# Performance work log

Measured on AMD Instinct MI355X. Metric: run time of the kernel, lower is better.

## Reference

```python
import jax, jax.numpy as jnp
import numpy as np

N_NODES = 100000
N_EDGES = 1600000
IN_FEATS, HIDDEN, OUT_MU, OUT_LV = 256, 128, 64, 64


def setup_inputs() -> dict:
    key = jax.random.key(0)
    ks = jax.random.split(key, 8)
    X = jax.random.normal(ks[0], (N_NODES, IN_FEATS), dtype=jnp.float32)
    edge_index = jax.random.randint(ks[1], (2, N_EDGES), 0, N_NODES, dtype=jnp.int64)
    def glorot(k, shape):
        lim = np.sqrt(6.0 / (shape[0] + shape[1])).astype(np.float32)
        return jax.random.uniform(k, shape, jnp.float32, -lim, lim)
    W1 = glorot(ks[2], (IN_FEATS, HIDDEN))
    b1 = jnp.zeros((HIDDEN,), jnp.float32)
    Wmu = glorot(ks[3], (HIDDEN, OUT_MU))
    bmu = jnp.zeros((OUT_MU,), jnp.float32)
    Wlv = glorot(ks[4], (HIDDEN, OUT_LV))
    blv = jnp.zeros((OUT_LV,), jnp.float32)
    return {"X": X, "edge_index": edge_index, "W1": W1, "b1": b1,
            "Wmu": Wmu, "bmu": bmu, "Wlv": Wlv, "blv": blv}


def _gcn_norm(edge_index, num_nodes):
    # Add self-loops (PyG GCNConv default) and compute symmetric normalization.
    loop = jnp.arange(num_nodes, dtype=edge_index.dtype)
    row = jnp.concatenate([edge_index[0], loop])  # source
    col = jnp.concatenate([edge_index[1], loop])  # target
    deg = jax.ops.segment_sum(jnp.ones_like(col, dtype=jnp.float32), col,
                              num_segments=num_nodes)
    dinv = jnp.where(deg > 0, jax.lax.rsqrt(deg), 0.0)
    norm = dinv[row] * dinv[col]  # [E+N]
    return row, col, norm


def _gcn_conv(x, W, b, row, col, norm, num_nodes):
    # Linear transform, then normalized sparse neighbor aggregation at targets.
    h = x @ W                                   # [N, F_out]
    msg = h[row] * norm[:, None]                # gather + scale, [E+N, F_out]
    out = jax.ops.segment_sum(msg, col, num_segments=num_nodes)
    return out + b


def reference(X, edge_index, W1, b1, Wmu, bmu, Wlv, blv):
    n = X.shape[0]
    row, col, norm = _gcn_norm(edge_index, n)
    H = jax.nn.relu(_gcn_conv(X, W1, b1, row, col, norm, n))
    mu = _gcn_conv(H, Wmu, bmu, row, col, norm, n)
    lv = _gcn_conv(H, Wlv, blv, row, col, norm, n)
    return (mu, lv)
```

## Files before the change

### kernel.cpp

```cpp
#include <hip/hip_runtime.h>
#include <hip/hip_bf16.h>
#include <cstdint>

#define N_FEATS_IN 256
#define HID 128
#define OUTF 64
#define SITEMS 8
#define NXCD 8

typedef __bf16 bf16x8 __attribute__((ext_vector_type(8)));
typedef __bf16 bf16x2 __attribute__((ext_vector_type(2)));
typedef float f32x4 __attribute__((ext_vector_type(4)));

__device__ __forceinline__ int xcc_id() {
  int x;
  asm volatile("s_getreg_b32 %0, hwreg(HW_REG_XCC_ID, 0, 32)" : "=s"(x));
  return x & (NXCD - 1);
}


__global__ __launch_bounds__(256) void count_deg_kernel(const int* __restrict__ ei, int E,
    int N, int* __restrict__ cnt8, int* __restrict__ erank) {
  int e = blockIdx.x * 256 + threadIdx.x;
  int x = xcc_id();
  if (e < E) {
    int c = ei[E + e];
    int lr = __hip_atomic_fetch_add(&cnt8[(size_t)x * N + c], 1,
                                    __ATOMIC_RELAXED, __HIP_MEMORY_SCOPE_WORKGROUP);
    erank[e] = lr | (x << 28);
  }
}

__global__ __launch_bounds__(256) void combine_kernel(int* __restrict__ cnt8,
    int* __restrict__ deg, float* __restrict__ dinv, int n) {
  int c = blockIdx.x * 256 + threadIdx.x;
  if (c < n) {
    int s = 0;
#pragma unroll
    for (int x = 0; x < NXCD; ++x) {
      int v = cnt8[(size_t)x * n + c];
      cnt8[(size_t)x * n + c] = s;
      s += v;
    }
    deg[c] = s;
    dinv[c] = rsqrtf((float)(s + 1));
  }
}


__global__ __launch_bounds__(256) void scan_part_kernel(const int* __restrict__ cnt, int n,
                                                        int* __restrict__ bsum) {
  __shared__ int ts[256];
  const int t = threadIdx.x;
  int base = (blockIdx.x * 256 + t) * SITEMS;
  int s = 0;
#pragma unroll
  for (int i = 0; i < SITEMS; ++i) {
    int idx = base + i;
    if (idx < n) s += cnt[idx];
  }
  ts[t] = s;
  __syncthreads();
  for (int off = 128; off > 0; off >>= 1) {
    if (t < off) ts[t] += ts[t + off];
    __syncthreads();
  }
  if (t == 0) bsum[blockIdx.x] = ts[0];
}

__global__ __launch_bounds__(256) void scan_bsum_kernel(int* __restrict__ bsum, int nb) {
  __shared__ int ts[256];
  const int t = threadIdx.x;
  int v = (t < nb) ? bsum[t] : 0;
  ts[t] = v;
  __syncthreads();
  for (int off = 1; off < 256; off <<= 1) {
    int u = (t >= off) ? ts[t - off] : 0;
    __syncthreads();
    ts[t] += u;
    __syncthreads();
  }
  if (t < nb) bsum[t] = ts[t] - v;
}

__global__ __launch_bounds__(256) void scan_final_kernel(const int* __restrict__ cnt, int n,
    const int* __restrict__ bsum, int* __restrict__ ptr) {
  __shared__ int ts[256];
  const int t = threadIdx.x;
  int base = (blockIdx.x * 256 + t) * SITEMS;
  int loc[SITEMS];
  int s = 0;
#pragma unroll
  for (int i = 0; i < SITEMS; ++i) {
    int idx = base + i;
    loc[i] = (idx < n) ? cnt[idx] : 0;
    s += loc[i];
  }
  ts[t] = s;
  __syncthreads();
  for (int off = 1; off < 256; off <<= 1) {
    int u = (t >= off) ? ts[t - off] : 0;
    __syncthreads();
    ts[t] += u;
    __syncthreads();
  }
  int run = bsum[blockIdx.x] + ts[t] - s;
#pragma unroll
  for (int i = 0; i < SITEMS; ++i) {
    int idx = base + i;
    if (idx < n) ptr[idx] = run;
    run += loc[i];
  }
  if (base < n && base + SITEMS >= n) ptr[n] = run;
}


__global__ __launch_bounds__(256) void fill_kernel(const int* __restrict__ ei, int E, int N,
    const int* __restrict__ ptr, const int* __restrict__ offs, const int* __restrict__ erank,
    const float* __restrict__ dinv, int2* __restrict__ erec) {
  int e = blockIdx.x * 256 + threadIdx.x;
  if (e < E) {
    int r = ei[e];
    int c = ei[E + e];
    int er = erank[e];
    int x = er >> 28;
    int lr = er & 0x0FFFFFFF;
    int pos = ptr[c] + offs[(size_t)x * N + c] + lr;
    int2 rec;
    rec.x = r;
    rec.y = __float_as_int(dinv[r] * dinv[c]);
    erec[pos] = rec;
  }
}


__global__ __launch_bounds__(256) void pack_all_kernel(const float* __restrict__ W1,
    const float* __restrict__ Wmu, const float* __restrict__ Wlv,
    __bf16* __restrict__ W1p, __bf16* __restrict__ Wcp) {
  int idx = blockIdx.x * 256 + threadIdx.x;
  if (idx < 32768) {
    int j = idx & 7, l = (idx >> 3) & 63, t = (idx >> 9) & 7, s = idx >> 12;
    int k = s * 32 + (l >> 4) * 8 + j;
    int n = t * 16 + (l & 15);
    W1p[idx] = (__bf16)W1[k * HID + n];
  } else if (idx < 49152) {
    int i2 = idx - 32768;
    int j = i2 & 7, l = (i2 >> 3) & 63, t = (i2 >> 9) & 7, s = i2 >> 12;
    int k = s * 32 + (l >> 4) * 8 + j;
    int g = t * 16 + (l & 15);
    float v = (g < OUTF) ? Wmu[k * OUTF + g] : Wlv[k * OUTF + (g - OUTF)];
    Wcp[i2] = (__bf16)v;
  }
}


__global__ __launch_bounds__(256) void gemm1_mfma(const float* __restrict__ X,
    const __bf16* __restrict__ Wp, __bf16* __restrict__ Yb, int nrows, int ntiles) {
  __shared__ __bf16 bs[32768];
  const int tid = threadIdx.x;
  {
    const float4* s4 = (const float4*)Wp;
    float4* d4 = (float4*)bs;
#pragma unroll
    for (int i = 0; i < 16; ++i) d4[tid + 256 * i] = s4[tid + 256 * i];
  }
  __syncthreads();
  const int lane = tid & 63;
  const int wave = tid >> 6;
  const int lm = lane & 15;
  const int q = lane >> 4;
  const bf16x8* bsv = (const bf16x8*)bs;

  for (int tile = blockIdx.x; tile < ntiles; tile += gridDim.x) {
    const int rb = tile * 128 + wave * 32;
    int r0 = min(rb + lm, nrows - 1);
    int r1 = min(rb + 16 + lm, nrows - 1);
    const float* x0 = X + (size_t)r0 * N_FEATS_IN + q * 8;
    const float* x1 = X + (size_t)r1 * N_FEATS_IN + q * 8;

    f32x4 acc[2][8];
#pragma unroll
    for (int m = 0; m < 2; ++m)
#pragma unroll
      for (int t = 0; t < 8; ++t) acc[m][t] = (f32x4)0.f;

#pragma unroll
    for (int s = 0; s < 8; ++s) {
      float4 u0 = ((const float4*)(x0 + s * 32))[0];
      float4 v0 = ((const float4*)(x0 + s * 32))[1];
      float4 u1 = ((const float4*)(x1 + s * 32))[0];
      float4 v1 = ((const float4*)(x1 + s * 32))[1];
      bf16x8 a0, a1;
      a0[0] = (__bf16)u0.x; a0[1] = (__bf16)u0.y; a0[2] = (__bf16)u0.z; a0[3] = (__bf16)u0.w;
      a0[4] = (__bf16)v0.x; a0[5] = (__bf16)v0.y; a0[6] = (__bf16)v0.z; a0[7] = (__bf16)v0.w;
      a1[0] = (__bf16)u1.x; a1[1] = (__bf16)u1.y; a1[2] = (__bf16)u1.z; a1[3] = (__bf16)u1.w;
      a1[4] = (__bf16)v1.x; a1[5] = (__bf16)v1.y; a1[6] = (__bf16)v1.z; a1[7] = (__bf16)v1.w;
#pragma unroll
      for (int t = 0; t < 8; ++t) {
        bf16x8 b = bsv[(s * 8 + t) * 64 + lane];
        acc[0][t] = __builtin_amdgcn_mfma_f32_16x16x32_bf16(a0, b, acc[0][t], 0, 0, 0);
        acc[1][t] = __builtin_amdgcn_mfma_f32_16x16x32_bf16(a1, b, acc[1][t], 0, 0, 0);
      }
    }
#pragma unroll
    for (int m = 0; m < 2; ++m) {
      int rowbase = rb + m * 16 + q * 4;
#pragma unroll
      for (int t = 0; t < 8; ++t) {
#pragma unroll
        for (int r = 0; r < 4; ++r) {
          int row = rowbase + r;
          if (row < nrows) Yb[(size_t)row * HID + t * 16 + lm] = (__bf16)acc[m][t][r];
        }
      }
    }
  }
}


__global__ __launch_bounds__(64) void agg_kernel(const __bf16* __restrict__ Fin,
    const int* __restrict__ ptr, const int2* __restrict__ erec,
    const float* __restrict__ dinv, const float* __restrict__ bias,
    __bf16* __restrict__ Fout, int do_relu) {
  const int c = blockIdx.x;
  const int t = threadIdx.x;
  const float d = dinv[c];
  bf16x2 sv = ((const bf16x2*)(Fin + (size_t)c * HID))[t];
  float ax = d * d * (float)sv[0];
  float ay = d * d * (float)sv[1];
  const int beg = ptr[c], end = ptr[c + 1];
  int e = beg;
  for (; e + 4 <= end; e += 4) {
    int2 p0 = erec[e], p1 = erec[e + 1], p2 = erec[e + 2], p3 = erec[e + 3];
    float n0 = __int_as_float(p0.y), n1 = __int_as_float(p1.y);
    float n2 = __int_as_float(p2.y), n3 = __int_as_float(p3.y);
    bf16x2 v0 = ((const bf16x2*)(Fin + (size_t)p0.x * HID))[t];
    bf16x2 v1 = ((const bf16x2*)(Fin + (size_t)p1.x * HID))[t];
    bf16x2 v2 = ((const bf16x2*)(Fin + (size_t)p2.x * HID))[t];
    bf16x2 v3 = ((const bf16x2*)(Fin + (size_t)p3.x * HID))[t];
    ax = fmaf(n0, (float)v0[0], ax); ay = fmaf(n0, (float)v0[1], ay);
    ax = fmaf(n1, (float)v1[0], ax); ay = fmaf(n1, (float)v1[1], ay);
    ax = fmaf(n2, (float)v2[0], ax); ay = fmaf(n2, (float)v2[1], ay);
    ax = fmaf(n3, (float)v3[0], ax); ay = fmaf(n3, (float)v3[1], ay);
  }
  for (; e < end; ++e) {
    int2 p = erec[e];
    float nn = __int_as_float(p.y);
    bf16x2 v = ((const bf16x2*)(Fin + (size_t)p.x * HID))[t];
    ax = fmaf(nn, (float)v[0], ax);
    ay = fmaf(nn, (float)v[1], ay);
  }
  if (do_relu) {
    ax = fmaxf(ax + bias[2 * t], 0.f);
    ay = fmaxf(ay + bias[2 * t + 1], 0.f);
  }
  bf16x2 o;
  o[0] = (__bf16)ax;
  o[1] = (__bf16)ay;
  ((bf16x2*)(Fout + (size_t)c * HID))[t] = o;
}


__global__ __launch_bounds__(256) void gemm2_mfma(const __bf16* __restrict__ Gb,
    const __bf16* __restrict__ Wp, const float* __restrict__ bmu,
    const float* __restrict__ blv, float* __restrict__ out, int nrows) {
  __shared__ __bf16 bs[16384];
  const int tid = threadIdx.x;
  {
    const float4* s4 = (const float4*)Wp;
    float4* d4 = (float4*)bs;
#pragma unroll
    for (int i = 0; i < 8; ++i) d4[tid + 256 * i] = s4[tid + 256 * i];
  }
  __syncthreads();
  const int lane = tid & 63;
  const int wave = tid >> 6;
  const int rb = blockIdx.x * 128 + wave * 32;
  const int lm = lane & 15;
  const int q = lane >> 4;
  const bf16x8* bsv = (const bf16x8*)bs;

  f32x4 acc[2][8];
#pragma unroll
  for (int m = 0; m < 2; ++m)
#pragma unroll
    for (int t = 0; t < 8; ++t) acc[m][t] = (f32x4)0.f;

  int r0 = min(rb + lm, nrows - 1);
  int r1 = min(rb + 16 + lm, nrows - 1);
  const __bf16* g0 = Gb + (size_t)r0 * HID + q * 8;
  const __bf16* g1 = Gb + (size_t)r1 * HID + q * 8;

#pragma unroll
  for (int s = 0; s < 4; ++s) {
    bf16x8 a0 = *(const bf16x8*)(g0 + s * 32);
    bf16x8 a1 = *(const bf16x8*)(g1 + s * 32);
#pragma unroll
    for (int t = 0; t < 8; ++t) {
      bf16x8 b = bsv[(s * 8 + t) * 64 + lane];
      acc[0][t] = __builtin_amdgcn_mfma_f32_16x16x32_bf16(a0, b, acc[0][t], 0, 0, 0);
      acc[1][t] = __builtin_amdgcn_mfma_f32_16x16x32_bf16(a1, b, acc[1][t], 0, 0, 0);
    }
  }
#pragma unroll
  for (int m = 0; m < 2; ++m) {
    int rowbase = rb + m * 16 + q * 4;
#pragma unroll
    for (int t = 0; t < 8; ++t) {
      int g = t * 16 + lm;
      float bv = (g < OUTF) ? bmu[g] : blv[g - OUTF];
      float* ob = (g < OUTF) ? (out + g) : (out + (size_t)nrows * OUTF + (g - OUTF));
#pragma unroll
      for (int r = 0; r < 4; ++r) {
        int row = rowbase + r;
        if (row < nrows) ob[(size_t)row * OUTF] = acc[m][t][r] + bv;
      }
    }
  }
}


extern "C" void kernel_launch(void* const* d_in, const int* in_sizes, int n_in,
                              void* d_out, int out_size, void* d_ws, size_t ws_size,
                              hipStream_t stream) {
  const float* X   = (const float*)d_in[0];
  const int*   ei  = (const int*)d_in[1];
  const float* W1  = (const float*)d_in[2];
  const float* b1  = (const float*)d_in[3];
  const float* Wmu = (const float*)d_in[4];
  const float* bmu = (const float*)d_in[5];
  const float* Wlv = (const float*)d_in[6];
  const float* blv = (const float*)d_in[7];
  float* out = (float*)d_out;

  const int N = in_sizes[0] / N_FEATS_IN;
  const int E = in_sizes[1] / 2;

  char* ws = (char*)d_ws;
  size_t off = 0;
  auto alloc = [&](size_t bytes) -> void* {
    void* p = ws + off;
    off += (bytes + 255) & ~(size_t)255;
    return p;
  };
  __bf16* Yb  = (__bf16*)alloc((size_t)N * HID * 2);
  __bf16* Hb  = (__bf16*)alloc((size_t)N * HID * 2);
  float* dinv = (float*)alloc((size_t)N * 4);
  int*   deg  = (int*)alloc((size_t)N * 4);
  int*   ptr  = (int*)alloc((size_t)(N + 1) * 4);
  int*   cnt8 = (int*)alloc((size_t)NXCD * N * 4);
  int*   erank = (int*)alloc((size_t)E * 4);
  int2*  erec = (int2*)alloc((size_t)E * 8);
  __bf16* W1p = (__bf16*)alloc(32768 * 2);
  __bf16* Wcp = (__bf16*)alloc(16384 * 2);
  int*   bsum = (int*)alloc(256 * 4);
  (void)ws_size; (void)n_in; (void)out_size;

  hipMemsetAsync(cnt8, 0, (size_t)NXCD * N * 4, stream);

  int ge = (E + 255) / 256;
  int gn = (N + 255) / 256;
  int nb = (N + 256 * SITEMS - 1) / (256 * SITEMS);
  count_deg_kernel<<<ge, 256, 0, stream>>>(ei, E, N, cnt8, erank);
  combine_kernel<<<gn, 256, 0, stream>>>(cnt8, deg, dinv, N);
  scan_part_kernel<<<nb, 256, 0, stream>>>(deg, N, bsum);
  scan_bsum_kernel<<<1, 256, 0, stream>>>(bsum, nb);
  scan_final_kernel<<<nb, 256, 0, stream>>>(deg, N, bsum, ptr);
  fill_kernel<<<ge, 256, 0, stream>>>(ei, E, N, ptr, cnt8, erank, dinv, erec);
  pack_all_kernel<<<192, 256, 0, stream>>>(W1, Wmu, Wlv, W1p, Wcp);

  int ntiles = (N + 127) / 128;
  int g1 = ntiles < 512 ? ntiles : 512;
  gemm1_mfma<<<g1, 256, 0, stream>>>(X, W1p, Yb, N, ntiles);
  agg_kernel<<<N, 64, 0, stream>>>(Yb, ptr, erec, dinv, b1, Hb, 1);
  agg_kernel<<<N, 64, 0, stream>>>(Hb, ptr, erec, dinv, b1, Yb, 0);
  gemm2_mfma<<<ntiles, 256, 0, stream>>>(Yb, Wcp, bmu, blv, out, N);
}
```

Before: 469.3 us.

## Shrink GEMM row tiles to 64, prefetch X rows, persist gemm2 blocks

Both MFMA GEMMs now give each wave 16 rows instead of 32, so a block covers 64 rows and there are twice as many tiles. gemm1 issues all 16 float4 loads of a row up front before converting and running the MFMAs, which puts more loads in flight. gemm2 becomes a grid-stride persistent kernel capped at 768 blocks and hoists the bias and output-offset setup out of the tile loop. The aim is better latency hiding and occupancy from fewer accumulators, at the cost of reusing each LDS B fragment across only one A fragment per load.

New measurement: 460.2 us. Within noise of the previous version (-1.9%).

```diff
diff --git a/kernel.cpp b/kernel.cpp
--- a/kernel.cpp
+++ b/kernel.cpp
@@ -16,6 +16,13 @@
   int x;
   asm volatile("s_getreg_b32 %0, hwreg(HW_REG_XCC_ID, 0, 32)" : "=s"(x));
   return x & (NXCD - 1);
+}
+
+__device__ __forceinline__ bf16x8 cvt8(float4 u, float4 v) {
+  bf16x8 a;
+  a[0] = (__bf16)u.x; a[1] = (__bf16)u.y; a[2] = (__bf16)u.z; a[3] = (__bf16)u.w;
+  a[4] = (__bf16)v.x; a[5] = (__bf16)v.y; a[6] = (__bf16)v.z; a[7] = (__bf16)v.w;
+  return a;
 }
 
 
@@ -172,46 +179,35 @@
   const bf16x8* bsv = (const bf16x8*)bs;
 
   for (int tile = blockIdx.x; tile < ntiles; tile += gridDim.x) {
-    const int rb = tile * 128 + wave * 32;
-    int r0 = min(rb + lm, nrows - 1);
-    int r1 = min(rb + 16 + lm, nrows - 1);
-    const float* x0 = X + (size_t)r0 * N_FEATS_IN + q * 8;
-    const float* x1 = X + (size_t)r1 * N_FEATS_IN + q * 8;
-
-    f32x4 acc[2][8];
-#pragma unroll
-    for (int m = 0; m < 2; ++m)
-#pragma unroll
-      for (int t = 0; t < 8; ++t) acc[m][t] = (f32x4)0.f;
-
+    const int row0 = tile * 64 + wave * 16;
+    const int r = min(row0 + lm, nrows - 1);
+    const float4* xp = (const float4*)(X + (size_t)r * N_FEATS_IN) + q * 2;
+
+    float4 xa[16];
 #pragma unroll
     for (int s = 0; s < 8; ++s) {
-      float4 u0 = ((const float4*)(x0 + s * 32))[0];
-      float4 v0 = ((const float4*)(x0 + s * 32))[1];
-      float4 u1 = ((const float4*)(x1 + s * 32))[0];
-      float4 v1 = ((const float4*)(x1 + s * 32))[1];
-      bf16x8 a0, a1;
-      a0[0] = (__bf16)u0.x; a0[1] = (__bf16)u0.y; a0[2] = (__bf16)u0.z; a0[3] = (__bf16)u0.w;
-      a0[4] = (__bf16)v0.x; a0[5] = (__bf16)v0.y; a0[6] = (__bf16)v0.z; a0[7] = (__bf16)v0.w;
-      a1[0] = (__bf16)u1.x; a1[1] = (__bf16)u1.y; a1[2] = (__bf16)u1.z; a1[3] = (__bf16)u1.w;
-      a1[4] = (__bf16)v1.x; a1[5] = (__bf16)v1.y; a1[6] = (__bf16)v1.z; a1[7] = (__bf16)v1.w;
-#pragma unroll
-      for (int t = 0; t < 8; ++t) {
-        bf16x8 b = bsv[(s * 8 + t) * 64 + lane];
-        acc[0][t] = __builtin_amdgcn_mfma_f32_16x16x32_bf16(a0, b, acc[0][t], 0, 0, 0);
-        acc[1][t] = __builtin_amdgcn_mfma_f32_16x16x32_bf16(a1, b, acc[1][t], 0, 0, 0);
-      }
-    }
-#pragma unroll
-    for (int m = 0; m < 2; ++m) {
-      int rowbase = rb + m * 16 + q * 4;
-#pragma unroll
-      for (int t = 0; t < 8; ++t) {
-#pragma unroll
-        for (int r = 0; r < 4; ++r) {
-          int row = rowbase + r;
-          if (row < nrows) Yb[(size_t)row * HID + t * 16 + lm] = (__bf16)acc[m][t][r];
-        }
+      xa[2 * s]     = xp[s * 8];
+      xa[2 * s + 1] = xp[s * 8 + 1];
+    }
+
+    f32x4 acc[8];
+#pragma unroll
+    for (int t = 0; t < 8; ++t) acc[t] = (f32x4)0.f;
+
+#pragma unroll
+    for (int s = 0; s < 8; ++s) {
+      bf16x8 a = cvt8(xa[2 * s], xa[2 * s + 1]);
+#pragma unroll
+      for (int t = 0; t < 8; ++t)
+        acc[t] = __builtin_amdgcn_mfma_f32_16x16x32_bf16(a, bsv[(s * 8 + t) * 64 + lane],
+                                                         acc[t], 0, 0, 0);
+    }
+#pragma unroll
+    for (int t = 0; t < 8; ++t) {
+#pragma unroll
+      for (int r2 = 0; r2 < 4; ++r2) {
+        int row = row0 + q * 4 + r2;
+        if (row < nrows) Yb[(size_t)row * HID + t * 16 + lm] = (__bf16)acc[t][r2];
       }
     }
   }
@@ -263,7 +259,7 @@
 
 __global__ __launch_bounds__(256) void gemm2_mfma(const __bf16* __restrict__ Gb,
     const __bf16* __restrict__ Wp, const float* __restrict__ bmu,
-    const float* __restrict__ blv, float* __restrict__ out, int nrows) {
+    const float* __restrict__ blv, float* __restrict__ out, int nrows, int ntiles) {
   __shared__ __bf16 bs[16384];
   const int tid = threadIdx.x;
   {
@@ -275,45 +271,47 @@
   __syncthreads();
   const int lane = tid & 63;
   const int wave = tid >> 6;
-  const int rb = blockIdx.x * 128 + wave * 32;
   const int lm = lane & 15;
   const int q = lane >> 4;
   const bf16x8* bsv = (const bf16x8*)bs;
 
-  f32x4 acc[2][8];
-#pragma unroll
-  for (int m = 0; m < 2; ++m)
-#pragma unroll
-    for (int t = 0; t < 8; ++t) acc[m][t] = (f32x4)0.f;
-
-  int r0 = min(rb + lm, nrows - 1);
-  int r1 = min(rb + 16 + lm, nrows - 1);
-  const __bf16* g0 = Gb + (size_t)r0 * HID + q * 8;
-  const __bf16* g1 = Gb + (size_t)r1 * HID + q * 8;
-
-#pragma unroll
-  for (int s = 0; s < 4; ++s) {
-    bf16x8 a0 = *(const bf16x8*)(g0 + s * 32);
-    bf16x8 a1 = *(const bf16x8*)(g1 + s * 32);
+  const int g = (lane & 15) * 1;
+  float bv[8];
+  size_t obase[8];
+#pragma unroll
+  for (int t = 0; t < 8; ++t) {
+    int col = t * 16 + (lane & 15);
+    bv[t] = (col < OUTF) ? bmu[col] : blv[col - OUTF];
+    obase[t] = (col < OUTF) ? (size_t)col : ((size_t)nrows * OUTF + (col - OUTF));
+  }
+  (void)g;
+
+  for (int tile = blockIdx.x; tile < ntiles; tile += gridDim.x) {
+    const int row0 = tile * 64 + wave * 16;
+    const int r = min(row0 + lm, nrows - 1);
+    const bf16x8* gp = (const bf16x8*)(Gb + (size_t)r * HID);
+
+    bf16x8 xa[4];
+#pragma unroll
+    for (int s = 0; s < 4; ++s) xa[s] = gp[s * 4 + q];
+
+    f32x4 acc[8];
+#pragma unroll
+    for (int t = 0; t < 8; ++t) acc[t] = (f32x4)0.f;
+
+#pragma unroll
+    for (int s = 0; s < 4; ++s) {
+#pragma unroll
+      for (int t = 0; t < 8; ++t)
+        acc[t] = __builtin_amdgcn_mfma_f32_16x16x32_bf16(xa[s], bsv[(s * 8 + t) * 64 + lane],
+                                                         acc[t], 0, 0, 0);
+    }
 #pragma unroll
     for (int t = 0; t < 8; ++t) {
-      bf16x8 b = bsv[(s * 8 + t) * 64 + lane];
-      acc[0][t] = __builtin_amdgcn_mfma_f32_16x16x32_bf16(a0, b, acc[0][t], 0, 0, 0);
-      acc[1][t] = __builtin_amdgcn_mfma_f32_16x16x32_bf16(a1, b, acc[1][t], 0, 0, 0);
-    }
-  }
-#pragma unroll
-  for (int m = 0; m < 2; ++m) {
-    int rowbase = rb + m * 16 + q * 4;
-#pragma unroll
-    for (int t = 0; t < 8; ++t) {
-      int g = t * 16 + lm;
-      float bv = (g < OUTF) ? bmu[g] : blv[g - OUTF];
-      float* ob = (g < OUTF) ? (out + g) : (out + (size_t)nrows * OUTF + (g - OUTF));
-#pragma unroll
-      for (int r = 0; r < 4; ++r) {
-        int row = rowbase + r;
-        if (row < nrows) ob[(size_t)row * OUTF] = acc[m][t][r] + bv;
+#pragma unroll
+      for (int r2 = 0; r2 < 4; ++r2) {
+        int row = row0 + q * 4 + r2;
+        if (row < nrows) out[obase[t] + (size_t)row * OUTF] = acc[t][r2] + bv[t];
       }
     }
   }
@@ -369,10 +367,11 @@
   fill_kernel<<<ge, 256, 0, stream>>>(ei, E, N, ptr, cnt8, erank, dinv, erec);
   pack_all_kernel<<<192, 256, 0, stream>>>(W1, Wmu, Wlv, W1p, Wcp);
 
-  int ntiles = (N + 127) / 128;
+  int ntiles = (N + 63) / 64;
   int g1 = ntiles < 512 ? ntiles : 512;
+  int g2 = ntiles < 768 ? ntiles : 768;
   gemm1_mfma<<<g1, 256, 0, stream>>>(X, W1p, Yb, N, ntiles);
   agg_kernel<<<N, 64, 0, stream>>>(Yb, ptr, erec, dinv, b1, Hb, 1);
   agg_kernel<<<N, 64, 0, stream>>>(Hb, ptr, erec, dinv, b1, Yb, 0);
-  gemm2_mfma<<<ntiles, 256, 0, stream>>>(Yb, Wcp, bmu, blv, out, N);
-}
+  gemm2_mfma<<<g2, 256, 0, stream>>>(Yb, Wcp, bmu, blv, out, N, ntiles);
+}
```
